# Kernel tuning notes

Measured on AMD Instinct MI355X. Metric: run time of the kernel, lower is better.

The kernel has to match this reference:

```python
import jax, jax.numpy as jnp
import numpy as np

B, S, DIM = 2, 2048, 2048
H = 16
Q_LORA, KV_LORA = 512, 512
D_NOPE, D_ROPE, D_V = 128, 64, 128
D_QK = D_NOPE + D_ROPE  # 192
SCALE = D_QK ** -0.5
EPS = 1e-6


def rmsnorm(x, w):
    return x * jax.lax.rsqrt(jnp.mean(x * x, axis=-1, keepdims=True) + EPS) * w


def apply_rope(x, cos, sin):
    # x: [B, S, h, d] with d even; cos/sin: [S, d//2] (complex-pair rotation)
    xs = x.reshape(*x.shape[:-1], -1, 2)
    x0, x1 = xs[..., 0], xs[..., 1]
    c = cos[None, :, None, :]
    s = sin[None, :, None, :]
    out = jnp.stack([x0 * c - x1 * s, x0 * s + x1 * c], axis=-1)
    return out.reshape(x.shape)


def setup_inputs() -> dict:
    key = jax.random.key(0)
    ks = jax.random.split(key, 8)
    std = 0.02
    x = jax.random.normal(ks[0], (B, S, DIM), dtype=jnp.float32)
    wq_a_w = jax.random.normal(ks[1], (DIM, Q_LORA), dtype=jnp.float32) * std
    wq_a_b = jnp.zeros((Q_LORA,), dtype=jnp.float32)
    q_norm_w = jnp.ones((Q_LORA,), dtype=jnp.float32)
    wq_b_w = jax.random.normal(ks[2], (Q_LORA, H * D_QK), dtype=jnp.float32) * std
    wkv_a_w = jax.random.normal(ks[3], (DIM, KV_LORA + D_ROPE), dtype=jnp.float32) * std
    wkv_a_b = jnp.zeros((KV_LORA + D_ROPE,), dtype=jnp.float32)
    kv_norm_w = jnp.ones((KV_LORA,), dtype=jnp.float32)
    wkv_b_w = jax.random.normal(ks[4], (KV_LORA, H * (D_NOPE + D_V)), dtype=jnp.float32) * std
    wo_w = jax.random.normal(ks[5], (H * D_V, DIM), dtype=jnp.float32) * std
    # rotary table: freqs_cis[t, i] = exp(1j * t * 10000^{-2i/d})
    inv_freq = 1.0 / (10000.0 ** (np.arange(0, D_ROPE, 2, dtype=np.float32) / D_ROPE))
    t = np.arange(S, dtype=np.float32)
    ang = np.outer(t, inv_freq)  # [S, D_ROPE//2]
    freqs_cos = jnp.asarray(np.cos(ang), dtype=jnp.float32)
    freqs_sin = jnp.asarray(np.sin(ang), dtype=jnp.float32)
    # causal mask (prefill): 0 on/below diagonal, -1e9 above
    mask = jnp.where(jnp.arange(S)[:, None] >= jnp.arange(S)[None, :], 0.0, -1e9).astype(jnp.float32)
    return {"x": x, "wq_a_w": wq_a_w, "wq_a_b": wq_a_b, "q_norm_w": q_norm_w,
            "wq_b_w": wq_b_w, "wkv_a_w": wkv_a_w, "wkv_a_b": wkv_a_b,
            "kv_norm_w": kv_norm_w, "wkv_b_w": wkv_b_w, "wo_w": wo_w,
            "freqs_cos": freqs_cos, "freqs_sin": freqs_sin, "mask": mask,
            "start_pos": 0}


def reference(x, wq_a_w, wq_a_b, q_norm_w, wq_b_w, wkv_a_w, wkv_a_b,
              kv_norm_w, wkv_b_w, wo_w, freqs_cos, freqs_sin, mask, start_pos):
    bsz, seqlen, _ = x.shape
    # low-rank Q: wq_b(q_norm(wq_a(x)))
    q = rmsnorm(x @ wq_a_w + wq_a_b, q_norm_w) @ wq_b_w
    q = q.reshape(bsz, seqlen, H, D_QK)
    q_nope, q_pe = q[..., :D_NOPE], q[..., D_NOPE:]
    q_pe = apply_rope(q_pe, freqs_cos, freqs_sin)
    # low-rank KV
    kv_full = x @ wkv_a_w + wkv_a_b
    kv, k_pe = kv_full[..., :KV_LORA], kv_full[..., KV_LORA:]
    k_pe = apply_rope(k_pe[:, :, None, :], freqs_cos, freqs_sin)  # [B,S,1,D_ROPE]
    kv = rmsnorm(kv, kv_norm_w) @ wkv_b_w
    kv = kv.reshape(bsz, seqlen, H, D_NOPE + D_V)
    k_nope, v = kv[..., :D_NOPE], kv[..., D_NOPE:]
    k = jnp.concatenate([k_nope, jnp.broadcast_to(k_pe, (bsz, seqlen, H, D_ROPE))], axis=-1)
    # prefill (start_pos=0): cache[:, :end_pos] == freshly written k, v
    q = jnp.concatenate([q_nope, q_pe], axis=-1)
    scores = jnp.einsum('bshd,bthd->bsht', q, k) * SCALE
    scores = scores + mask[None, :, None, :]
    attn = jax.nn.softmax(scores.astype(jnp.float32), axis=-1).astype(q.dtype)
    out = jnp.einsum('bsht,bthd->bshd', attn, v)
    return out.reshape(bsz, seqlen, H * D_V) @ wo_w
```

## Files before the change

### kernel.cpp

```cpp
#include <hip/hip_runtime.h>
#include <hip/hip_bf16.h>

typedef unsigned short u16;
typedef unsigned int u32;
typedef __attribute__((ext_vector_type(8))) __bf16 bf16x8;
typedef __attribute__((ext_vector_type(4))) float f32x4;
typedef __attribute__((ext_vector_type(4))) u32 u32x4;
typedef __attribute__((ext_vector_type(2))) u32 u32x2;

#define S_LEN 2048
#define BF16_ONE 0x3F80u

__device__ __forceinline__ float b2f(u16 u) {
  union { unsigned u; float f; } v; v.u = ((unsigned)u) << 16; return v.f;
}
__device__ __forceinline__ u16 f2b(float f) {
  union { float f; unsigned u; } v; v.f = f;
  unsigned r = v.u + 0x7fffu + ((v.u >> 16) & 1u);
  return (u16)(r >> 16);
}
__device__ __forceinline__ u32 cvt_pk_bf16(float a, float b) {
  u32 r;
  asm("v_cvt_pk_bf16_f32 %0, %1, %2" : "=v"(r) : "v"(a), "v"(b));
  return r;
}

__device__ __forceinline__ void glds16(const u16* g, u16* l) {
  __builtin_amdgcn_global_load_lds((const __attribute__((address_space(1))) void*)g,
                                   (__attribute__((address_space(3))) void*)l, 16, 0, 0);
}

__device__ __forceinline__ bool probe_f32(const u16* p) { return p[0] != (u16)BF16_ONE; }

struct CvtDesc {
  const void* src[7];
  u16* dst[7];
  int cum[8];
};
__global__ __launch_bounds__(256) void cvt_batch(CvtDesc d, const u16* __restrict__ probe,
                                                 int total) {
  int i = blockIdx.x * 256 + threadIdx.x;
  if (i >= total) return;
  int t = 0;
#pragma unroll
  for (int k = 1; k < 7; ++k) t += (i >= d.cum[k]);
  int li = i - d.cum[t];
  if (probe_f32(probe)) {
    const float* s = (const float*)d.src[t] + (long)li * 8;
    u16 tmp[8];
#pragma unroll
    for (int j = 0; j < 8; ++j) tmp[j] = f2b(s[j]);
    *(u32x4*)(d.dst[t] + (long)li * 8) = *(const u32x4*)tmp;
  } else {
    *(u32x4*)(d.dst[t] + (long)li * 8) = ((const u32x4*)d.src[t])[li];
  }
}

struct TrDesc {
  const void* in[5];
  u16* out[5];
  int R[5], C[5];
  int tcum[6];
  float scale[5];
};
__global__ __launch_bounds__(256) void transpose_batch(TrDesc d,
                                                       const u16* __restrict__ probe) {
  __shared__ u16 tile[32][33];
  int bid = blockIdx.x;
  int t = 0;
#pragma unroll
  for (int k = 1; k < 5; ++k) t += (bid >= d.tcum[k]);
  int rem = bid - d.tcum[t];
  const int R = d.R[t], C = d.C[t];
  const int tilesX = C >> 5;
  const int bx = rem % tilesX, by = rem / tilesX;
  const int c0 = bx * 32, r0 = by * 32;
  const int tx = threadIdx.x, ty = threadIdx.y;
  const float sc = d.scale[t];
  if (probe_f32(probe)) {
    const float* inf = (const float*)d.in[t];
#pragma unroll
    for (int i = 0; i < 4; ++i)
      tile[ty + i * 8][tx] = f2b(inf[(long)(r0 + ty + i * 8) * C + c0 + tx] * sc);
  } else {
    const u16* inb = (const u16*)d.in[t];
#pragma unroll
    for (int i = 0; i < 4; ++i)
      tile[ty + i * 8][tx] = f2b(b2f(inb[(long)(r0 + ty + i * 8) * C + c0 + tx]) * sc);
  }
  __syncthreads();
  u16* outp = d.out[t];
#pragma unroll
  for (int i = 0; i < 4; ++i)
    outp[(long)(c0 + ty + i * 8) * R + r0 + tx] = tile[tx][ty + i * 8];
}

__global__ __launch_bounds__(256) void transpose_v(const u16* __restrict__ kvb,
                                                   u16* __restrict__ vt) {
  __shared__ u16 tile[32][33];
  int s0 = blockIdx.x * 32, d0 = blockIdx.y * 32, bh = blockIdx.z;
  int b = bh >> 4, h = bh & 15;
  int tx = threadIdx.x, ty = threadIdx.y;
#pragma unroll
  for (int i = 0; i < 4; ++i)
    tile[ty + i * 8][tx] =
        kvb[((long)b * S_LEN + s0 + ty + i * 8) * 4096 + h * 256 + 128 + d0 + tx];
  __syncthreads();
#pragma unroll
  for (int i = 0; i < 4; ++i)
    vt[((long)bh * 128 + d0 + ty + i * 8) * S_LEN + s0 + tx] = tile[tx][ty + i * 8];
}

template <int MT>
__global__ __launch_bounds__(256) void gemm_bt(const u16* __restrict__ A,
                                               const u16* __restrict__ Bt,
                                               const u16* __restrict__ bias,
                                               void* __restrict__ Cv,
                                               int M, int N, int K,
                                               const u16* __restrict__ oprobe) {
  constexpr int MI = MT / 32;
  __shared__ u16 As[2][MT * 32];
  __shared__ u16 Bs[2][128 * 32];
  const int tid = threadIdx.x;
  const int lane = tid & 63;
  const int w = tid >> 6;
  const int quad = lane >> 4;
  const int l16 = lane & 15;
  const int m0 = blockIdx.y * MT;
  const int n0 = blockIdx.x * 128;
  const int wm = (w >> 1) * (MT / 2);
  const int wn = (w & 1) * 64;

  const f32x4 zero = {0.f, 0.f, 0.f, 0.f};
  f32x4 acc[MI][4];
#pragma unroll
  for (int i = 0; i < MI; ++i)
#pragma unroll
    for (int j = 0; j < 4; ++j) acc[i][j] = zero;

  auto stage = [&](int k0, int buf) {
#pragma unroll
    for (int cc = 0; cc < MT * 4; cc += 256) {
      int j = cc + tid, ar = j >> 2, ak = ((j & 3) ^ (ar & 3)) * 8;
      glds16(A + (long)(m0 + ar) * K + k0 + ak, As[buf] + j * 8);
    }
#pragma unroll
    for (int cc = 0; cc < 512; cc += 256) {
      int j = cc + tid, br = j >> 2, bk = ((j & 3) ^ (br & 3)) * 8;
      int bn = n0 + br; if (bn > N - 1) bn = N - 1;
      glds16(Bt + (long)bn * K + k0 + bk, Bs[buf] + j * 8);
    }
  };

  const int nk = K >> 5;
  stage(0, 0);
  for (int t = 0; t < nk; ++t) {
    __syncthreads();
    if (t + 1 < nk) stage((t + 1) << 5, (t + 1) & 1);
    const u16* as = As[t & 1];
    const u16* bs = Bs[t & 1];
    bf16x8 af[MI], bfr[4];
#pragma unroll
    for (int mi = 0; mi < MI; ++mi)
      af[mi] = *(const bf16x8*)(as + (wm + mi * 16 + l16) * 32 +
                                ((quad ^ (l16 & 3)) * 8));
#pragma unroll
    for (int ni = 0; ni < 4; ++ni)
      bfr[ni] = *(const bf16x8*)(bs + (wn + ni * 16 + l16) * 32 +
                                 ((quad ^ (l16 & 3)) * 8));
#pragma unroll
    for (int mi = 0; mi < MI; ++mi)
#pragma unroll
      for (int ni = 0; ni < 4; ++ni)
        acc[mi][ni] = __builtin_amdgcn_mfma_f32_16x16x32_bf16(af[mi], bfr[ni],
                                                              acc[mi][ni], 0, 0, 0);
  }

  u16* C = (u16*)Cv;
  float* Cf = (float*)Cv;
  const bool of32 = oprobe && probe_f32(oprobe);
#pragma unroll
  for (int ni = 0; ni < 4; ++ni) {
    int col = n0 + wn + ni * 16 + l16;
    if (col >= N) continue;
    float bv = bias ? b2f(bias[col]) : 0.0f;
#pragma unroll
    for (int mi = 0; mi < MI; ++mi) {
      int row = m0 + wm + mi * 16 + quad * 4;
#pragma unroll
      for (int r = 0; r < 4; ++r) {
        float val = acc[mi][ni][r] + bv;
        if (of32) Cf[(long)(row + r) * N + col] = val;
        else      C[(long)(row + r) * N + col] = f2b(val);
      }
    }
  }
}

__global__ __launch_bounds__(256) void rmsnorm512(const u16* __restrict__ in, int in_stride,
                                                  const u16* __restrict__ w,
                                                  u16* __restrict__ out, int out_stride) {
  __shared__ float red[4];
  int row = blockIdx.x, tid = threadIdx.x;
  const u16* x = in + (long)row * in_stride;
  float v0 = b2f(x[tid]), v1 = b2f(x[tid + 256]);
  float ss = v0 * v0 + v1 * v1;
#pragma unroll
  for (int off = 1; off < 64; off <<= 1) ss += __shfl_xor(ss, off);
  if ((tid & 63) == 0) red[tid >> 6] = ss;
  __syncthreads();
  float tot = red[0] + red[1] + red[2] + red[3];
  float r = rsqrtf(tot * (1.0f / 512.0f) + 1e-6f);
  u16* y = out + (long)row * out_stride;
  y[tid] = f2b(v0 * r * b2f(w[tid]));
  y[tid + 256] = f2b(v1 * r * b2f(w[tid + 256]));
}

__global__ __launch_bounds__(256) void rope_q_kernel(u16* __restrict__ q,
                                                     const u16* __restrict__ fc,
                                                     const u16* __restrict__ fs) {
  int i = blockIdx.x * 256 + threadIdx.x;
  int pair = i & 31;
  int h = (i >> 5) & 15;
  int row = i >> 9;
  int pos = row & (S_LEN - 1);
  long base = (long)row * 3072 + h * 192 + 128 + pair * 2;
  float x0 = b2f(q[base]), x1 = b2f(q[base + 1]);
  float c = b2f(fc[pos * 32 + pair]), s = b2f(fs[pos * 32 + pair]);
  q[base] = f2b(x0 * c - x1 * s);
  q[base + 1] = f2b(x0 * s + x1 * c);
}

__global__ __launch_bounds__(256) void rope_k_kernel(const u16* __restrict__ kva,
                                                     u16* __restrict__ kpe,
                                                     const u16* __restrict__ fc,
                                                     const u16* __restrict__ fs) {
  int i = blockIdx.x * 256 + threadIdx.x;
  int pair = i & 31;
  int row = i >> 5;
  int pos = row & (S_LEN - 1);
  long sb = (long)row * 576 + 512 + pair * 2;
  float x0 = b2f(kva[sb]), x1 = b2f(kva[sb + 1]);
  float c = b2f(fc[pos * 32 + pair]), s = b2f(fs[pos * 32 + pair]);
  kpe[(long)row * 64 + pair * 2] = f2b(x0 * c - x1 * s);
  kpe[(long)row * 64 + pair * 2 + 1] = f2b(x0 * s + x1 * c);
}

__global__ __launch_bounds__(256, 2) void mla_attn(const u16* __restrict__ q,
                                                   const u16* __restrict__ kvb,
                                                   const u16* __restrict__ vt,
                                                   const u16* __restrict__ kpe,
                                                   u16* __restrict__ o) {
  __shared__ u16 Ks[2][64 * 192];
  __shared__ u16 Vts[128 * 64];
  const int tid = threadIdx.x;
  const int w = tid >> 6;
  const int lane = tid & 63;
  const int quad = lane >> 4;
  const int l16 = lane & 15;
  const int bh = blockIdx.x;
  const int b = bh >> 4, h = bh & 15;
  const long rowbase = (long)b * S_LEN;
  const f32x4 zero = {0.f, 0.f, 0.f, 0.f};

  auto stage_k = [&](int t0s, u16* dst) {
#pragma unroll
    for (int tt = 0; tt < 6; ++tt) {
      int j = tt * 256 + tid;
      int r = j / 24, csw = j % 24;
      int c = csw ^ (r & 7);
      const u16* src = (c < 16)
                           ? (kvb + (rowbase + t0s + r) * 4096 + h * 256 + c * 8)
                           : (kpe + (rowbase + t0s + r) * 64 + (c - 16) * 8);
      glds16(src, dst + j * 8);
    }
  };
  auto stage_v = [&](int t0s) {
#pragma unroll
    for (int tt = 0; tt < 4; ++tt) {
      int j = tt * 256 + tid;
      int d = j >> 3, c = (j & 7) ^ (d & 7);
      glds16(vt + ((long)bh * 128 + d) * S_LEN + t0s + c * 8, Vts + j * 8);
    }
  };

  const int srcA = (((quad & 1) << 1) | (quad >> 1)) * 16 + l16;
  const int srcB = srcA ^ 16;
  const bool lowq = quad < 2;
  const int p = quad & 1;

  const int yy = blockIdx.y;
  const int jt = (yy < 8) ? yy : 23 - yy;
  const int q0 = jt * 128;
  const int ntiles = 2 * jt + 2;
  const int rowlo = q0 + w * 32;

  const u16* qrowA = q + (rowbase + rowlo + l16) * 3072 + h * 192;
  const u16* qrowB = qrowA + 16 * 3072;
  bf16x8 qfA[6], qfB[6];
#pragma unroll
  for (int kk = 0; kk < 6; ++kk) {
    qfA[kk] = *(const bf16x8*)(qrowA + kk * 32 + quad * 8);
    qfB[kk] = *(const bf16x8*)(qrowB + kk * 32 + quad * 8);
  }

  float mA = -INFINITY, mB = -INFINITY;
  float lA = 0.f, lB = 0.f;
  f32x4 oA[8], oB[8];
#pragma unroll
  for (int i = 0; i < 8; ++i) { oA[i] = zero; oB[i] = zero; }

  auto finish_half = [&](f32x4* s, float& m_r, float& l_r, f32x4* oacc,
                         int lim, bool needmask, bf16x8& ap0, bf16x8& ap1) {
    if (needmask) {
#pragma unroll
      for (int g = 0; g < 4; ++g)
#pragma unroll
        for (int r = 0; r < 4; ++r)
          s[g][r] = (g * 16 + r > lim) ? -1e30f : s[g][r];
    }
    float mx0 = fmaxf(fmaxf(s[0][0], s[0][1]), fmaxf(s[0][2], s[0][3]));
    float mx1 = fmaxf(fmaxf(s[1][0], s[1][1]), fmaxf(s[1][2], s[1][3]));
    float mx2 = fmaxf(fmaxf(s[2][0], s[2][1]), fmaxf(s[2][2], s[2][3]));
    float mx3 = fmaxf(fmaxf(s[3][0], s[3][1]), fmaxf(s[3][2], s[3][3]));
    float vmax = fmaxf(fmaxf(mx0, mx1), fmaxf(mx2, mx3));
    vmax = fmaxf(vmax, __shfl_xor(vmax, 16));
    vmax = fmaxf(vmax, __shfl_xor(vmax, 32));

    if (!__all(vmax <= m_r + 8.0f)) {
      float mnew = fmaxf(m_r, vmax);
      float alpha = __expf(m_r - mnew);
      m_r = mnew;
      l_r *= alpha;
      float al0 = __shfl(alpha, (lane & 48) | (quad * 4 + 0));
      float al1 = __shfl(alpha, (lane & 48) | (quad * 4 + 1));
      float al2 = __shfl(alpha, (lane & 48) | (quad * 4 + 2));
      float al3 = __shfl(alpha, (lane & 48) | (quad * 4 + 3));
#pragma unroll
      for (int nt = 0; nt < 8; ++nt) {
        f32x4 tt = oacc[nt];
        tt[0] *= al0; tt[1] *= al1; tt[2] *= al2; tt[3] *= al3;
        oacc[nt] = tt;
      }
    }

    float e00 = __expf(s[0][0] - m_r), e01 = __expf(s[0][1] - m_r);
    float e02 = __expf(s[0][2] - m_r), e03 = __expf(s[0][3] - m_r);
    float e10 = __expf(s[1][0] - m_r), e11 = __expf(s[1][1] - m_r);
    float e12 = __expf(s[1][2] - m_r), e13 = __expf(s[1][3] - m_r);
    float e20 = __expf(s[2][0] - m_r), e21 = __expf(s[2][1] - m_r);
    float e22 = __expf(s[2][2] - m_r), e23 = __expf(s[2][3] - m_r);
    float e30 = __expf(s[3][0] - m_r), e31 = __expf(s[3][1] - m_r);
    float e32 = __expf(s[3][2] - m_r), e33 = __expf(s[3][3] - m_r);
    l_r += ((e00 + e01) + (e02 + e03)) + ((e10 + e11) + (e12 + e13)) +
           ((e20 + e21) + (e22 + e23)) + ((e30 + e31) + (e32 + e33));
    u32 pk0x = cvt_pk_bf16(e00, e01), pk0y = cvt_pk_bf16(e02, e03);
    u32 pk1x = cvt_pk_bf16(e10, e11), pk1y = cvt_pk_bf16(e12, e13);
    u32 pk2x = cvt_pk_bf16(e20, e21), pk2y = cvt_pk_bf16(e22, e23);
    u32 pk3x = cvt_pk_bf16(e30, e31), pk3y = cvt_pk_bf16(e32, e33);

    u32 a0c = p ? pk1x : pk0x, a1c = p ? pk1y : pk0y;
    u32 a2c = p ? pk3x : pk2x, a3c = p ? pk3y : pk2y;
    u32 b0c = p ? pk0x : pk1x, b1c = p ? pk0y : pk1y;
    u32 b2c = p ? pk2x : pk3x, b3c = p ? pk2y : pk3y;
    u32 A0 = __shfl(a0c, srcA), A1 = __shfl(a1c, srcA);
    u32 A2 = __shfl(a2c, srcA), A3 = __shfl(a3c, srcA);
    u32 B0 = __shfl(b0c, srcB), B1 = __shfl(b1c, srcB);
    u32 B2 = __shfl(b2c, srcB), B3 = __shfl(b3c, srcB);
    u32x4 w0 = {lowq ? A0 : B0, lowq ? A1 : B1, lowq ? B0 : A0, lowq ? B1 : A1};
    u32x4 w1 = {lowq ? A2 : B2, lowq ? A3 : B3, lowq ? B2 : A2, lowq ? B3 : A3};
    ap0 = __builtin_bit_cast(bf16x8, w0);
    ap1 = __builtin_bit_cast(bf16x8, w1);
  };

  stage_k(0, Ks[0]);

  for (int t = 0; t < ntiles; ++t) {
    __syncthreads();
    stage_v(t * 64);
    if (t + 1 < ntiles) stage_k((t + 1) * 64, Ks[(t + 1) & 1]);
    const int t0 = t * 64;
    const bool active = (rowlo + 31 >= t0);
    bf16x8 apA0, apA1, apB0, apB1;
    if (active) {
      const u16* ks = Ks[t & 1];
      f32x4 sA[4] = {zero, zero, zero, zero};
      f32x4 sB[4] = {zero, zero, zero, zero};
      __builtin_amdgcn_s_setprio(1);
#pragma unroll
      for (int kk = 0; kk < 6; ++kk) {
        const int csw = ((kk * 4 + quad) ^ (l16 & 7)) * 8;
#pragma unroll
        for (int g = 0; g < 4; ++g) {
          bf16x8 kf = *(const bf16x8*)(ks + (g * 16 + l16) * 192 + csw);
          sA[g] = __builtin_amdgcn_mfma_f32_16x16x32_bf16(kf, qfA[kk], sA[g], 0, 0, 0);
          sB[g] = __builtin_amdgcn_mfma_f32_16x16x32_bf16(kf, qfB[kk], sB[g], 0, 0, 0);
        }
      }
      __builtin_amdgcn_s_setprio(0);

      const bool nmA = (t0 + 63 > rowlo);
      const bool nmB = (t0 + 63 > rowlo + 16);
      const int limA = rowlo + l16 - t0 - quad * 4;
      finish_half(sA, mA, lA, oA, limA, nmA, apA0, apA1);
      finish_half(sB, mB, lB, oB, limA + 16, nmB, apB0, apB1);
    }
    __syncthreads();
    if (active) {
      __builtin_amdgcn_s_setprio(1);
#pragma unroll
      for (int nt = 0; nt < 8; ++nt) {
        bf16x8 bv0 = *(const bf16x8*)(Vts + (nt * 16 + l16) * 64 +
                                      ((quad ^ (l16 & 7)) * 8));
        bf16x8 bv1 = *(const bf16x8*)(Vts + (nt * 16 + l16) * 64 +
                                      (((4 + quad) ^ (l16 & 7)) * 8));
        oA[nt] = __builtin_amdgcn_mfma_f32_16x16x32_bf16(apA0, bv0, oA[nt], 0, 0, 0);
        oA[nt] = __builtin_amdgcn_mfma_f32_16x16x32_bf16(apA1, bv1, oA[nt], 0, 0, 0);
        oB[nt] = __builtin_amdgcn_mfma_f32_16x16x32_bf16(apB0, bv0, oB[nt], 0, 0, 0);
        oB[nt] = __builtin_amdgcn_mfma_f32_16x16x32_bf16(apB1, bv1, oB[nt], 0, 0, 0);
      }
      __builtin_amdgcn_s_setprio(0);
    }
  }

  auto write_half = [&](float l_r, f32x4* oacc, long orow) {
    float ls = l_r;
    ls += __shfl_xor(ls, 16);
    ls += __shfl_xor(ls, 32);
    float i0 = __fdividef(1.0f, __shfl(ls, (lane & 48) | (quad * 4 + 0)));
    float i1 = __fdividef(1.0f, __shfl(ls, (lane & 48) | (quad * 4 + 1)));
    float i2 = __fdividef(1.0f, __shfl(ls, (lane & 48) | (quad * 4 + 2)));
    float i3 = __fdividef(1.0f, __shfl(ls, (lane & 48) | (quad * 4 + 3)));
#pragma unroll
    for (int nt = 0; nt < 8; ++nt) {
      o[(orow + 0) * 2048 + h * 128 + nt * 16 + l16] = f2b(oacc[nt][0] * i0);
      o[(orow + 1) * 2048 + h * 128 + nt * 16 + l16] = f2b(oacc[nt][1] * i1);
      o[(orow + 2) * 2048 + h * 128 + nt * 16 + l16] = f2b(oacc[nt][2] * i2);
      o[(orow + 3) * 2048 + h * 128 + nt * 16 + l16] = f2b(oacc[nt][3] * i3);
    }
  };
  const long orowA = rowbase + rowlo + quad * 4;
  write_half(lA, oA, orowA);
  write_half(lB, oB, orowA + 16);
}

extern "C" void kernel_launch(void* const* d_in, const int* in_sizes, int n_in,
                              void* d_out, int out_size, void* d_ws, size_t ws_size,
                              hipStream_t stream) {
  const void* x_raw    = d_in[0];
  const void* wqa_raw  = d_in[1];
  const void* wqab_raw = d_in[2];
  const void* qnw_raw  = d_in[3];
  const void* wqb_raw  = d_in[4];
  const void* wkva_raw = d_in[5];
  const void* wkvab_raw= d_in[6];
  const void* kvnw_raw = d_in[7];
  const void* wkvb_raw = d_in[8];
  const void* wo_raw   = d_in[9];
  const void* fc_raw   = d_in[10];
  const void* fs_raw   = d_in[11];
  const u16* probe = (const u16*)qnw_raw;
  const float SC = 0.07216878364870323f;

  char* ws = (char*)d_ws;
  size_t off = 0;
  auto alloc = [&](size_t n) { void* p = ws + off; off += (n + 255) & ~(size_t)255; return p; };
  u16* xb     = (u16*)alloc(4096ull * 2048 * 2);
  u16* fcb    = (u16*)alloc(2048ull * 32 * 2);
  u16* fsb    = (u16*)alloc(2048ull * 32 * 2);
  u16* wqab_b = (u16*)alloc(512ull * 2);
  u16* qnw_b  = (u16*)alloc(512ull * 2);
  u16* wkvab_b= (u16*)alloc(576ull * 2);
  u16* kvnw_b = (u16*)alloc(512ull * 2);
  u16* wqa_t  = (u16*)alloc(512ull * 2048 * 2);
  u16* wqb_t  = (u16*)alloc(3072ull * 512 * 2);
  u16* wkva_t = (u16*)alloc(576ull * 2048 * 2);
  u16* wkvb_t = (u16*)alloc(4096ull * 512 * 2);
  u16* wo_t   = (u16*)alloc(2048ull * 2048 * 2);
  u16* qa     = (u16*)alloc(4096ull * 512 * 2);
  u16* qbuf   = (u16*)alloc(4096ull * 3072 * 2);
  u16* kva    = (u16*)alloc(4096ull * 576 * 2);
  u16* kvn    = (u16*)alloc(4096ull * 512 * 2);
  u16* kpe    = (u16*)alloc(4096ull * 64 * 2);
  u16* kvb    = (u16*)alloc(4096ull * 4096 * 2);
  u16* vtb    = (u16*)alloc(32ull * 128 * 2048 * 2);
  u16* attn   = (u16*)alloc(4096ull * 2048 * 2);

  CvtDesc cd;
  const void* csrc[7] = {x_raw, fc_raw, fs_raw, wqab_raw, qnw_raw, wkvab_raw, kvnw_raw};
  u16* cdst[7] = {xb, fcb, fsb, wqab_b, qnw_b, wkvab_b, kvnw_b};
  long cn[7] = {4096l * 2048, 2048l * 32, 2048l * 32, 512, 512, 576, 512};
  int cum = 0;
  for (int i = 0; i < 7; ++i) {
    cd.src[i] = csrc[i]; cd.dst[i] = cdst[i];
    cd.cum[i] = cum; cum += (int)(cn[i] / 8);
  }
  cd.cum[7] = cum;
  cvt_batch<<<(cum + 255) / 256, 256, 0, stream>>>(cd, probe, cum);

  TrDesc td;
  const void* tin[5] = {wqa_raw, wqb_raw, wkva_raw, wkvb_raw, wo_raw};
  u16* tout[5] = {wqa_t, wqb_t, wkva_t, wkvb_t, wo_t};
  int tR[5] = {2048, 512, 2048, 512, 2048};
  int tC[5] = {512, 3072, 576, 4096, 2048};
  float tsc[5] = {1.0f, SC, 1.0f, 1.0f, 1.0f};
  int tcum = 0;
  for (int i = 0; i < 5; ++i) {
    td.in[i] = tin[i]; td.out[i] = tout[i];
    td.R[i] = tR[i]; td.C[i] = tC[i]; td.scale[i] = tsc[i];
    td.tcum[i] = tcum; tcum += (tR[i] / 32) * (tC[i] / 32);
  }
  td.tcum[5] = tcum;
  transpose_batch<<<tcum, dim3(32, 8), 0, stream>>>(td, probe);

  gemm_bt<64><<<dim3(4, 64), 256, 0, stream>>>(xb, wqa_t, wqab_b, qa, 4096, 512, 2048, nullptr);
  rmsnorm512<<<4096, 256, 0, stream>>>(qa, 512, qnw_b, qa, 512);
  gemm_bt<128><<<dim3(24, 32), 256, 0, stream>>>(qa, wqb_t, nullptr, qbuf, 4096, 3072, 512, nullptr);
  rope_q_kernel<<<8192, 256, 0, stream>>>(qbuf, fcb, fsb);

  gemm_bt<64><<<dim3(5, 64), 256, 0, stream>>>(xb, wkva_t, wkvab_b, kva, 4096, 576, 2048, nullptr);
  rmsnorm512<<<4096, 256, 0, stream>>>(kva, 576, kvnw_b, kvn, 512);
  rope_k_kernel<<<512, 256, 0, stream>>>(kva, kpe, fcb, fsb);
  gemm_bt<128><<<dim3(32, 32), 256, 0, stream>>>(kvn, wkvb_t, nullptr, kvb, 4096, 4096, 512, nullptr);
  transpose_v<<<dim3(64, 4, 32), dim3(32, 8), 0, stream>>>(kvb, vtb);

  mla_attn<<<dim3(32, 16), 256, 0, stream>>>(qbuf, kvb, vtb, kpe, attn);

  gemm_bt<128><<<dim3(16, 32), 256, 0, stream>>>(attn, wo_t, nullptr, d_out, 4096, 2048, 2048, probe);
}
```

Baseline: 433.9 us.

## Split attention KV loop across two warp groups with LDS softmax merge

The attention block grows from 256 to 512 threads. Two groups of four warps each process alternating 64-key tiles for the same 128 query rows, so each group runs half as many loop iterations. At the end the second group writes its partial O accumulators and max/sum statistics to shared memory, and the first group merges them with a flash-decoding style rescale before writing the output. This adds parallelism per block, at the cost of double the LDS buffers, occupancy of one block per CU, and an extra merge step.

```diff
diff --git a/kernel.cpp b/kernel.cpp
--- a/kernel.cpp
+++ b/kernel.cpp
@@ -246,15 +246,17 @@
   kpe[(long)row * 64 + pair * 2 + 1] = f2b(x0 * s + x1 * c);
 }
 
-__global__ __launch_bounds__(256, 2) void mla_attn(const u16* __restrict__ q,
+__global__ __launch_bounds__(512, 1) void mla_attn(const u16* __restrict__ q,
                                                    const u16* __restrict__ kvb,
                                                    const u16* __restrict__ vt,
                                                    const u16* __restrict__ kpe,
                                                    u16* __restrict__ o) {
-  __shared__ u16 Ks[2][64 * 192];
-  __shared__ u16 Vts[128 * 64];
+  __shared__ u16 Ks[2][2][64 * 192];
+  __shared__ u16 Vts[2][128 * 64];
   const int tid = threadIdx.x;
   const int w = tid >> 6;
+  const int g = w >> 2;
+  const int sw = w & 3;
   const int lane = tid & 63;
   const int quad = lane >> 4;
   const int l16 = lane & 15;
@@ -265,8 +267,8 @@
 
   auto stage_k = [&](int t0s, u16* dst) {
 #pragma unroll
-    for (int tt = 0; tt < 6; ++tt) {
-      int j = tt * 256 + tid;
+    for (int tt = 0; tt < 3; ++tt) {
+      int j = tt * 512 + tid;
       int r = j / 24, csw = j % 24;
       int c = csw ^ (r & 7);
       const u16* src = (c < 16)
@@ -275,12 +277,12 @@
       glds16(src, dst + j * 8);
     }
   };
-  auto stage_v = [&](int t0s) {
-#pragma unroll
-    for (int tt = 0; tt < 4; ++tt) {
-      int j = tt * 256 + tid;
+  auto stage_v = [&](int t0s, u16* dst) {
+#pragma unroll
+    for (int tt = 0; tt < 2; ++tt) {
+      int j = tt * 512 + tid;
       int d = j >> 3, c = (j & 7) ^ (d & 7);
-      glds16(vt + ((long)bh * 128 + d) * S_LEN + t0s + c * 8, Vts + j * 8);
+      glds16(vt + ((long)bh * 128 + d) * S_LEN + t0s + c * 8, dst + j * 8);
     }
   };
 
@@ -292,8 +294,8 @@
   const int yy = blockIdx.y;
   const int jt = (yy < 8) ? yy : 23 - yy;
   const int q0 = jt * 128;
-  const int ntiles = 2 * jt + 2;
-  const int rowlo = q0 + w * 32;
+  const int ns = jt + 1;
+  const int rowlo = q0 + sw * 32;
 
   const u16* qrowA = q + (rowbase + rowlo + l16) * 3072 + h * 192;
   const u16* qrowB = qrowA + 16 * 3072;
@@ -314,10 +316,10 @@
                          int lim, bool needmask, bf16x8& ap0, bf16x8& ap1) {
     if (needmask) {
 #pragma unroll
-      for (int g = 0; g < 4; ++g)
+      for (int gg = 0; gg < 4; ++gg)
 #pragma unroll
         for (int r = 0; r < 4; ++r)
-          s[g][r] = (g * 16 + r > lim) ? -1e30f : s[g][r];
+          s[gg][r] = (gg * 16 + r > lim) ? -1e30f : s[gg][r];
     }
     float mx0 = fmaxf(fmaxf(s[0][0], s[0][1]), fmaxf(s[0][2], s[0][3]));
     float mx1 = fmaxf(fmaxf(s[1][0], s[1][1]), fmaxf(s[1][2], s[1][3]));
@@ -373,17 +375,22 @@
     ap1 = __builtin_bit_cast(bf16x8, w1);
   };
 
-  stage_k(0, Ks[0]);
-
-  for (int t = 0; t < ntiles; ++t) {
+  stage_k(0, Ks[0][0]);
+  stage_k(64, Ks[0][1]);
+
+  for (int i = 0; i < ns; ++i) {
     __syncthreads();
-    stage_v(t * 64);
-    if (t + 1 < ntiles) stage_k((t + 1) * 64, Ks[(t + 1) & 1]);
-    const int t0 = t * 64;
+    stage_v((2 * i) * 64, Vts[0]);
+    stage_v((2 * i + 1) * 64, Vts[1]);
+    if (i + 1 < ns) {
+      stage_k((2 * i + 2) * 64, Ks[(i + 1) & 1][0]);
+      stage_k((2 * i + 3) * 64, Ks[(i + 1) & 1][1]);
+    }
+    const int t0 = (2 * i + g) * 64;
     const bool active = (rowlo + 31 >= t0);
     bf16x8 apA0, apA1, apB0, apB1;
     if (active) {
-      const u16* ks = Ks[t & 1];
+      const u16* ks = Ks[i & 1][g];
       f32x4 sA[4] = {zero, zero, zero, zero};
       f32x4 sB[4] = {zero, zero, zero, zero};
       __builtin_amdgcn_s_setprio(1);
@@ -391,10 +398,10 @@
       for (int kk = 0; kk < 6; ++kk) {
         const int csw = ((kk * 4 + quad) ^ (l16 & 7)) * 8;
 #pragma unroll
-        for (int g = 0; g < 4; ++g) {
-          bf16x8 kf = *(const bf16x8*)(ks + (g * 16 + l16) * 192 + csw);
-          sA[g] = __builtin_amdgcn_mfma_f32_16x16x32_bf16(kf, qfA[kk], sA[g], 0, 0, 0);
-          sB[g] = __builtin_amdgcn_mfma_f32_16x16x32_bf16(kf, qfB[kk], sB[g], 0, 0, 0);
+        for (int gg = 0; gg < 4; ++gg) {
+          bf16x8 kf = *(const bf16x8*)(ks + (gg * 16 + l16) * 192 + csw);
+          sA[gg] = __builtin_amdgcn_mfma_f32_16x16x32_bf16(kf, qfA[kk], sA[gg], 0, 0, 0);
+          sB[gg] = __builtin_amdgcn_mfma_f32_16x16x32_bf16(kf, qfB[kk], sB[gg], 0, 0, 0);
         }
       }
       __builtin_amdgcn_s_setprio(0);
@@ -407,12 +414,13 @@
     }
     __syncthreads();
     if (active) {
+      const u16* vs = Vts[g];
       __builtin_amdgcn_s_setprio(1);
 #pragma unroll
       for (int nt = 0; nt < 8; ++nt) {
-        bf16x8 bv0 = *(const bf16x8*)(Vts + (nt * 16 + l16) * 64 +
+        bf16x8 bv0 = *(const bf16x8*)(vs + (nt * 16 + l16) * 64 +
                                       ((quad ^ (l16 & 7)) * 8));
-        bf16x8 bv1 = *(const bf16x8*)(Vts + (nt * 16 + l16) * 64 +
+        bf16x8 bv1 = *(const bf16x8*)(vs + (nt * 16 + l16) * 64 +
                                       (((4 + quad) ^ (l16 & 7)) * 8));
         oA[nt] = __builtin_amdgcn_mfma_f32_16x16x32_bf16(apA0, bv0, oA[nt], 0, 0, 0);
         oA[nt] = __builtin_amdgcn_mfma_f32_16x16x32_bf16(apA1, bv1, oA[nt], 0, 0, 0);
@@ -423,25 +431,56 @@
     }
   }
 
-  auto write_half = [&](float l_r, f32x4* oacc, long orow) {
-    float ls = l_r;
-    ls += __shfl_xor(ls, 16);
-    ls += __shfl_xor(ls, 32);
-    float i0 = __fdividef(1.0f, __shfl(ls, (lane & 48) | (quad * 4 + 0)));
-    float i1 = __fdividef(1.0f, __shfl(ls, (lane & 48) | (quad * 4 + 1)));
-    float i2 = __fdividef(1.0f, __shfl(ls, (lane & 48) | (quad * 4 + 2)));
-    float i3 = __fdividef(1.0f, __shfl(ls, (lane & 48) | (quad * 4 + 3)));
+  float lsA = lA; lsA += __shfl_xor(lsA, 16); lsA += __shfl_xor(lsA, 32);
+  float lsB = lB; lsB += __shfl_xor(lsB, 16); lsB += __shfl_xor(lsB, 32);
+
+  float* zone = (float*)&Ks[0][0][0];
+  float* mlz = zone + 16384;
+  if (g == 1) {
+    float* zp0 = zone + ((sw * 2 + 0) * 64 + lane) * 32;
+    float* zp1 = zone + ((sw * 2 + 1) * 64 + lane) * 32;
 #pragma unroll
     for (int nt = 0; nt < 8; ++nt) {
-      o[(orow + 0) * 2048 + h * 128 + nt * 16 + l16] = f2b(oacc[nt][0] * i0);
-      o[(orow + 1) * 2048 + h * 128 + nt * 16 + l16] = f2b(oacc[nt][1] * i1);
-      o[(orow + 2) * 2048 + h * 128 + nt * 16 + l16] = f2b(oacc[nt][2] * i2);
-      o[(orow + 3) * 2048 + h * 128 + nt * 16 + l16] = f2b(oacc[nt][3] * i3);
-    }
-  };
-  const long orowA = rowbase + rowlo + quad * 4;
-  write_half(lA, oA, orowA);
-  write_half(lB, oB, orowA + 16);
+      *(f32x4*)(zp0 + nt * 4) = oA[nt];
+      *(f32x4*)(zp1 + nt * 4) = oB[nt];
+    }
+    mlz[((sw * 2 + 0) * 64 + lane) * 2 + 0] = mA;
+    mlz[((sw * 2 + 0) * 64 + lane) * 2 + 1] = lsA;
+    mlz[((sw * 2 + 1) * 64 + lane) * 2 + 0] = mB;
+    mlz[((sw * 2 + 1) * 64 + lane) * 2 + 1] = lsB;
+  }
+  __syncthreads();
+  if (g == 0) {
+    auto merge_write = [&](float m_r, float ls, f32x4* oacc, int hz) {
+      const float* zp = zone + ((sw * 2 + hz) * 64 + lane) * 32;
+      float mo = mlz[((sw * 2 + hz) * 64 + lane) * 2 + 0];
+      float lo = mlz[((sw * 2 + hz) * 64 + lane) * 2 + 1];
+      float mm = fmaxf(m_r, mo);
+      float aA = __expf(m_r - mm);
+      float aB = __expf(mo - mm);
+      float lt = ls * aA + lo * aB;
+      float sAl = __fdividef(aA, lt);
+      float sBl = __fdividef(aB, lt);
+      float sa[4], sb[4];
+#pragma unroll
+      for (int r = 0; r < 4; ++r) {
+        int src = (lane & 48) | (quad * 4 + r);
+        sa[r] = __shfl(sAl, src);
+        sb[r] = __shfl(sBl, src);
+      }
+      const long orow = rowbase + q0 + sw * 32 + hz * 16 + quad * 4;
+#pragma unroll
+      for (int nt = 0; nt < 8; ++nt) {
+        f32x4 op = *(const f32x4*)(zp + nt * 4);
+#pragma unroll
+        for (int r = 0; r < 4; ++r)
+          o[(orow + r) * 2048 + h * 128 + nt * 16 + l16] =
+              f2b(oacc[nt][r] * sa[r] + op[r] * sb[r]);
+      }
+    };
+    merge_write(mA, lsA, oA, 0);
+    merge_write(mB, lsB, oB, 1);
+  }
 }
 
 extern "C" void kernel_launch(void* const* d_in, const int* in_sizes, int n_in,
@@ -524,7 +563,7 @@
   gemm_bt<128><<<dim3(32, 32), 256, 0, stream>>>(kvn, wkvb_t, nullptr, kvb, 4096, 4096, 512, nullptr);
   transpose_v<<<dim3(64, 4, 32), dim3(32, 8), 0, stream>>>(kvb, vtb);
 
-  mla_attn<<<dim3(32, 16), 256, 0, stream>>>(qbuf, kvb, vtb, kpe, attn);
+  mla_attn<<<dim3(32, 16), 512, 0, stream>>>(qbuf, kvb, vtb, kpe, attn);
 
   gemm_bt<128><<<dim3(16, 32), 256, 0, stream>>>(attn, wo_t, nullptr, d_out, 4096, 2048, 2048, probe);
 }
```

New measurement: 426.5 us. Within noise of the previous version (-1.7%).
